# Performance work log

Measured on AMD Instinct MI355X. Metric: run time of the kernel, lower is better.

Reference implementation:

```python
import jax, jax.numpy as jnp
import numpy as np

H, O, E, V = 128, 128, 512, 34
B, T, L = 64, 2048, 256


def _lstm(x, wih, whh, bih, bhh):
    # x: [T, B, Din] -> outputs [T, B, H]; PyTorch gate order i, f, g, o
    n = whh.shape[1]
    h0 = jnp.zeros((x.shape[1], n), x.dtype)
    b = bih + bhh
    def step(carry, xt):
        h, c = carry
        g = xt @ wih.T + h @ whh.T + b
        i, f, gg, o = jnp.split(g, 4, axis=-1)
        c = jax.nn.sigmoid(f) * c + jax.nn.sigmoid(i) * jnp.tanh(gg)
        h = jax.nn.sigmoid(o) * jnp.tanh(c)
        return (h, c), h
    _, ys = jax.lax.scan(step, (h0, h0), x)
    return ys


def _conv1d_s2(x, w, b):
    # x: [B, Cin, T], w: [Cout, Cin, 2], kernel=2 stride=2 valid
    y = jax.lax.conv_general_dilated(x, w, (2,), 'VALID', dimension_numbers=('NCH', 'OIH', 'NCH'))
    return y + b[None, :, None]


def setup_inputs():
    key = jax.random.key(0)
    ctr = [0]
    def mk(shape, s=0.05):
        ctr[0] += 1
        return jax.random.normal(jax.random.fold_in(key, ctr[0]), shape, dtype=jnp.float32) * s
    inp = {}
    inp['utter'] = mk((B, T, 40), 1.0)
    inp['targets'] = jax.random.randint(jax.random.fold_in(key, 999), (B, L), 0, V)
    inp['wih_f'] = mk((4 * H, 40)); inp['whh_f'] = mk((4 * H, H)); inp['bih_f'] = mk((4 * H,)); inp['bhh_f'] = mk((4 * H,))
    inp['wih_r'] = mk((4 * H, 40)); inp['whh_r'] = mk((4 * H, H)); inp['bih_r'] = mk((4 * H,)); inp['bhh_r'] = mk((4 * H,))
    inp['c1w'] = mk((H, 2 * H, 2)); inp['c1b'] = mk((H,))
    inp['wih1'] = mk((4 * H, H)); inp['whh1'] = mk((4 * H, H)); inp['bih1'] = mk((4 * H,)); inp['bhh1'] = mk((4 * H,))
    inp['c2w'] = mk((H, H, 2)); inp['c2b'] = mk((H,))
    inp['wih2'] = mk((4 * H, H)); inp['whh2'] = mk((4 * H, H)); inp['bih2'] = mk((4 * H,)); inp['bhh2'] = mk((4 * H,))
    inp['kw'] = mk((O, H)); inp['kb'] = mk((O,)); inp['vw'] = mk((O, H)); inp['vb'] = mk((O,))
    inp['wihd'] = mk((4 * O, O + E)); inp['whhd'] = mk((4 * O, O)); inp['bihd'] = mk((4 * O,)); inp['bhhd'] = mk((4 * O,))
    inp['w1'] = mk((V, O)); inp['b1'] = mk((V,)); inp['w2'] = mk((V, O)); inp['b2'] = mk((V,))
    inp['w3'] = mk((V, V)); inp['b3'] = mk((V,))
    inp['emb'] = mk((V, E), 1.0)
    inp['sh0'] = mk((B, O)); inp['sc0'] = mk((B, O))
    return inp


def _forward(utter, targets, wih_f, whh_f, bih_f, bhh_f, wih_r, whh_r, bih_r, bhh_r,
             c1w, c1b, wih1, whh1, bih1, bhh1, c2w, c2b, wih2, whh2, bih2, bhh2,
             kw, kb, vw, vb, wihd, whhd, bihd, bhhd, w1, b1, w2, b2, w3, b3,
             emb, sh0, sc0):
    # ---- Listener (encoder) ----
    x = jnp.transpose(utter, (1, 0, 2))            # [T, B, 40]
    fwd = _lstm(x, wih_f, whh_f, bih_f, bhh_f)
    bwd = _lstm(x[::-1], wih_r, whh_r, bih_r, bhh_r)[::-1]
    h = jnp.concatenate([fwd, bwd], axis=-1)       # [T, B, 2H]
    h = jnp.transpose(h, (1, 2, 0))                # [B, 2H, T]
    h = _conv1d_s2(h, c1w, c1b)                    # [B, H, T/2]
    h = jnp.transpose(h, (2, 0, 1))                # [T/2, B, H]
    h = _lstm(h, wih1, whh1, bih1, bhh1)
    h = jnp.transpose(h, (1, 2, 0))
    h = _conv1d_s2(h, c2w, c2b)                    # [B, H, T/4]
    h = jnp.transpose(h, (2, 0, 1))
    h = _lstm(h, wih2, whh2, bih2, bhh2)
    h = jnp.transpose(h, (1, 0, 2))                # [B, T/4, H]
    hk = h @ kw.T + kb                              # [B, T/4, O]
    hv = h @ vw.T + vb
    # ---- Speller (decoder) ----
    ys = jnp.transpose(emb[targets], (1, 0, 2))[:-1]   # [L-1, B, E]
    mask = jnp.ones((utter.shape[0], hk.shape[1]), utter.dtype)  # all full-length
    bd = bihd + bhhd
    def step(carry, y_in):
        c, sh, sc = carry
        g = jnp.concatenate([y_in, c], axis=1) @ wihd.T + sh @ whhd.T + bd
        i, f, gg, o = jnp.split(g, 4, axis=-1)
        sc_n = jax.nn.sigmoid(f) * sc + jax.nn.sigmoid(i) * jnp.tanh(gg)
        sh_n = jax.nn.sigmoid(o) * jnp.tanh(sc_n)
        # NOTE: original attends with the cell state sc (faithful to source)
        att = jax.nn.softmax(jnp.einsum('btd,bd->bt', hk, sc_n), axis=1) * mask
        att = att / jnp.sum(att, axis=1, keepdims=True)
        c_n = jnp.einsum('bt,btd->bd', att, hv)
        out = jax.nn.relu(sh_n @ w1.T + b1 + c_n @ w2.T + b2)
        out = jax.nn.softmax(out @ w3.T + b3, axis=1)
        return (c_n, sh_n, sc_n), out
    c0 = jnp.zeros_like(sh0)
    _, preds = jax.lax.scan(step, (c0, sh0, sc0), ys)
    return jnp.transpose(preds, (1, 0, 2))         # [B, L-1, V]


def reference(utter, targets, wih_f, whh_f, bih_f, bhh_f, wih_r, whh_r, bih_r, bhh_r,
              c1w, c1b, wih1, whh1, bih1, bhh1, c2w, c2b, wih2, whh2, bih2, bhh2,
              kw, kb, vw, vb, wihd, whhd, bihd, bhhd, w1, b1, w2, b2, w3, b3,
              emb, sh0, sc0):
    return _forward(utter, targets, wih_f, whh_f, bih_f, bhh_f, wih_r, whh_r, bih_r, bhh_r,
                    c1w, c1b, wih1, whh1, bih1, bhh1, c2w, c2b, wih2, whh2, bih2, bhh2,
                    kw, kb, vw, vb, wihd, whhd, bihd, bhhd, w1, b1, w2, b2, w3, b3,
                    emb, sh0, sc0)
```

## Files before the change

### kernel.cpp

```cpp
#include <hip/hip_runtime.h>

typedef _Float16 half_t;
typedef _Float16 __attribute__((ext_vector_type(2))) half2_t;

__device__ __forceinline__ float fdot2_(half2_t a, half2_t b, float c) {
#if __has_builtin(__builtin_amdgcn_fdot2)
    return __builtin_amdgcn_fdot2(a, b, c, false);
#else
    return c + (float)a[0] * (float)b[0] + (float)a[1] * (float)b[1];
#endif
}
__device__ __forceinline__ half2_t h2(float a, float b) {
    half2_t r; r[0] = (half_t)a; r[1] = (half_t)b; return r;
}
__device__ __forceinline__ half2_t bc2(unsigned int u) {
    return __builtin_bit_cast(half2_t, u);
}
__device__ __forceinline__ unsigned int pk2(float a, float b) {
    return __builtin_bit_cast(unsigned int, h2(a, b));
}
__device__ __forceinline__ float sigm(float x) { return 1.0f / (1.0f + __expf(-x)); }
__device__ __forceinline__ float tanh_(float x) { return 1.0f - 2.0f / (1.0f + __expf(2.0f * x)); }
__device__ __forceinline__ unsigned int packbf2(float a, float b) {
    unsigned int ua = __float_as_uint(a);
    ua = (ua + 0x7fffu + ((ua >> 16) & 1u)) >> 16;
    unsigned int ub = __float_as_uint(b);
    ub = (ub + 0x7fffu + ((ub >> 16) & 1u)) >> 16;
    return ua | (ub << 16);
}
__device__ __forceinline__ float blo(unsigned int u) { return __uint_as_float(u << 16); }
__device__ __forceinline__ float bhi(unsigned int u) { return __uint_as_float(u & 0xffff0000u); }

__global__ __launch_bounds__(512, 1) void lstm1_k(
    const float* __restrict__ utter,
    const float* __restrict__ wih_f, const float* __restrict__ whh_f,
    const float* __restrict__ bih_f, const float* __restrict__ bhh_f,
    const float* __restrict__ wih_r, const float* __restrict__ whh_r,
    const float* __restrict__ bih_r, const float* __restrict__ bhh_r,
    unsigned short* __restrict__ Hf, unsigned short* __restrict__ Hr)
{
    const int tid = threadIdx.x;
    const int b   = blockIdx.x & 63;
    const int dir = blockIdx.x >> 6;
    const float* wih = dir ? wih_r : wih_f;
    const float* whh = dir ? whh_r : whh_f;
    const float* bih = dir ? bih_r : bih_f;
    const float* bhh = dir ? bhh_r : bhh_f;
    unsigned short* Hout = dir ? Hr : Hf;

    __shared__ float acts[512];
    __shared__ __align__(16) half_t h_h[128];
    __shared__ __align__(16) half_t x2[2][8][48];
    __shared__ __align__(16) float ring[8][128];

    const int j = tid;
    const int gt = tid >> 7;
    unsigned int wr2[64];
    {
        const float4* wp = reinterpret_cast<const float4*>(whh + j * 128);
#pragma unroll
        for (int m = 0; m < 32; ++m) {
            float4 v = wp[m];
            wr2[2 * m]     = pk2(v.x, v.y);
            wr2[2 * m + 1] = pk2(v.z, v.w);
        }
    }
    unsigned int wx2[20];
    {
        const float4* xp = reinterpret_cast<const float4*>(wih + j * 40);
#pragma unroll
        for (int q = 0; q < 10; ++q) {
            float4 v = xp[q];
            wx2[2 * q]     = pk2(v.x, v.y);
            wx2[2 * q + 1] = pk2(v.z, v.w);
        }
    }
    const float bias = bih[j] + bhh[j];
    float c = 0.0f;
    if (tid < 128) h_h[tid] = (half_t)0.0f;
    const int xs = tid / 40, xc = tid % 40;
    if (tid < 320) {
        int tt0 = dir ? (2047 - xs) : xs;
        x2[0][xs][xc] = (half_t)utter[((size_t)b * 2048 + tt0) * 40 + xc];
    }
    __syncthreads();

    for (int tc = 0; tc < 2048; tc += 8) {
        const int ph = (tc >> 3) & 1;
        float xreg = 0.0f;
        if (tid < 320) {
            int tn = tc + 8 + xs; if (tn > 2047) tn = 2047;
            int ttn = dir ? (2047 - tn) : tn;
            xreg = utter[((size_t)b * 2048 + ttn) * 40 + xc];
        }
#pragma unroll
        for (int s = 0; s < 8; ++s) {
            float g0 = bias, g1 = 0.f, g2 = 0.f, g3 = 0.f;
            {
                const uint4* x4p = reinterpret_cast<const uint4*>(&x2[ph][s][0]);
#pragma unroll
                for (int q = 0; q < 5; ++q) {
                    uint4 u = x4p[q];
                    g0 = fdot2_(bc2(wx2[4 * q]),     bc2(u.x), g0);
                    g1 = fdot2_(bc2(wx2[4 * q + 1]), bc2(u.y), g1);
                    g2 = fdot2_(bc2(wx2[4 * q + 2]), bc2(u.z), g2);
                    g3 = fdot2_(bc2(wx2[4 * q + 3]), bc2(u.w), g3);
                }
                const uint4* h4p = reinterpret_cast<const uint4*>(h_h);
#pragma unroll
                for (int q = 0; q < 16; ++q) {
                    uint4 u = h4p[q];
                    g0 = fdot2_(bc2(wr2[4 * q]),     bc2(u.x), g0);
                    g1 = fdot2_(bc2(wr2[4 * q + 1]), bc2(u.y), g1);
                    g2 = fdot2_(bc2(wr2[4 * q + 2]), bc2(u.z), g2);
                    g3 = fdot2_(bc2(wr2[4 * q + 3]), bc2(u.w), g3);
                }
            }
            float g = (g0 + g1) + (g2 + g3);
            acts[j] = (gt == 2) ? tanh_(g) : sigm(g);
            __syncthreads();
            if (s == 7 && tid < 320)
                x2[ph ^ 1][xs][xc] = (half_t)xreg;
            if (tid < 128) {
                float i_ = acts[tid];
                float f_ = acts[128 + tid];
                float g_ = acts[256 + tid];
                float o_ = acts[384 + tid];
                c = f_ * c + i_ * g_;
                float hh = o_ * tanh_(c);
                h_h[tid] = (half_t)hh;
                ring[s][tid] = hh;
            }
            __syncthreads();
        }
        {
            int s2 = tid >> 6, pr = tid & 63;
            int t = tc + s2;
            int tt = dir ? (2047 - t) : t;
            unsigned int v = pk2(ring[s2][2 * pr], ring[s2][2 * pr + 1]);
            reinterpret_cast<unsigned int*>(Hout)[((size_t)tt * 64 + b) * 64 + pr] = v;
        }
    }
}

__global__ __launch_bounds__(512, 1) void lstm_k(
    const unsigned short* __restrict__ Ph,
    const float* __restrict__ whh,
    void* __restrict__ Hout, int T, int outHalf)
{
    const int tid = threadIdx.x;
    const int b = blockIdx.x;
    const int j = tid;
    const int gt = tid >> 7;
    __shared__ float acts[512];
    __shared__ __align__(16) half_t h_h[128];
    __shared__ __align__(16) float ring[8][128];
    unsigned int wr2[64];
    {
        const float4* wp = reinterpret_cast<const float4*>(whh + j * 128);
#pragma unroll
        for (int m = 0; m < 32; ++m) {
            float4 v = wp[m];
            wr2[2 * m]     = pk2(v.x, v.y);
            wr2[2 * m + 1] = pk2(v.z, v.w);
        }
    }
    float c = 0.0f;
    if (tid < 128) h_h[tid] = (half_t)0.0f;
    const size_t pbase = (size_t)b * T;
    float pcur[8], pnext[8];
#pragma unroll
    for (int s = 0; s < 8; ++s)
        pcur[s] = (float)__builtin_bit_cast(half_t, Ph[(pbase + s) * 512 + j]);
    __syncthreads();

    for (int tc = 0; tc < T; tc += 8) {
#pragma unroll
        for (int s = 0; s < 8; ++s) {
            int tn = tc + 8 + s; if (tn > T - 1) tn = T - 1;
            pnext[s] = (float)__builtin_bit_cast(half_t, Ph[(pbase + tn) * 512 + j]);
        }
#pragma unroll
        for (int s = 0; s < 8; ++s) {
            float g0 = pcur[s], g1 = 0.f, g2 = 0.f, g3 = 0.f;
            const uint4* h4p = reinterpret_cast<const uint4*>(h_h);
#pragma unroll
            for (int q = 0; q < 16; ++q) {
                uint4 u = h4p[q];
                g0 = fdot2_(bc2(wr2[4 * q]),     bc2(u.x), g0);
                g1 = fdot2_(bc2(wr2[4 * q + 1]), bc2(u.y), g1);
                g2 = fdot2_(bc2(wr2[4 * q + 2]), bc2(u.z), g2);
                g3 = fdot2_(bc2(wr2[4 * q + 3]), bc2(u.w), g3);
            }
            float g = (g0 + g1) + (g2 + g3);
            acts[j] = (gt == 2) ? tanh_(g) : sigm(g);
            __syncthreads();
            if (tid < 128) {
                float i_ = acts[tid];
                float f_ = acts[128 + tid];
                float g_ = acts[256 + tid];
                float o_ = acts[384 + tid];
                c = f_ * c + i_ * g_;
                float hh = o_ * tanh_(c);
                h_h[tid] = (half_t)hh;
                ring[s][tid] = hh;
            }
            __syncthreads();
        }
        {
            int s2 = tid >> 6, pr = tid & 63;
            int t = tc + s2;
            if (outHalf) {
                unsigned int v = pk2(ring[s2][2 * pr], ring[s2][2 * pr + 1]);
                reinterpret_cast<unsigned int*>(Hout)[((size_t)t * 64 + b) * 64 + pr] = v;
            } else {
                float2 v = make_float2(ring[s2][2 * pr], ring[s2][2 * pr + 1]);
                *reinterpret_cast<float2*>(
                    &reinterpret_cast<float*>(Hout)[((size_t)t * 64 + b) * 128 + 2 * pr]) = v;
            }
        }
#pragma unroll
        for (int s = 0; s < 8; ++s) pcur[s] = pnext[s];
    }
}

template <int CIN>
__global__ __launch_bounds__(128) void conv_k(
    const unsigned short* __restrict__ HA, const unsigned short* __restrict__ HB,
    const float* __restrict__ W, const float* __restrict__ bias,
    float* __restrict__ out, int Tout)
{
    __shared__ __align__(16) float xin[64 * CIN];
    const int b = blockIdx.x;
    const int t0 = blockIdx.y * 32;
    const int tid = threadIdx.x;
    for (int idx = tid; idx < 64 * CIN; idx += 128) {
        int tl = idx / CIN, ci = idx % CIN;
        int tau = t0 * 2 + tl;
        unsigned short u;
        if constexpr (CIN == 256) {
            u = (ci < 128) ? HA[(size_t)tau * 8192 + b * 128 + ci]
                           : HB[(size_t)tau * 8192 + b * 128 + (ci - 128)];
        } else {
            u = HA[(size_t)tau * 8192 + b * 128 + ci];
        }
        xin[idx] = (float)__builtin_bit_cast(half_t, u);
    }
    __syncthreads();
    const int co = tid;
    float acc[32];
#pragma unroll
    for (int u = 0; u < 32; ++u) acc[u] = 0.0f;
    const float4* Wrow4 = reinterpret_cast<const float4*>(W + (size_t)co * 2 * CIN);
    const float4* xin4 = reinterpret_cast<const float4*>(xin);
    for (int c4 = 0; c4 < CIN / 4; ++c4) {
        float4 wA = Wrow4[2 * c4];
        float4 wB = Wrow4[2 * c4 + 1];
#pragma unroll
        for (int u = 0; u < 32; ++u) {
            float4 x0 = xin4[(2 * u) * (CIN / 4) + c4];
            float4 x1 = xin4[(2 * u + 1) * (CIN / 4) + c4];
            acc[u] += wA.x * x0.x + wA.y * x1.x + wA.z * x0.y + wA.w * x1.y
                    + wB.x * x0.z + wB.y * x1.z + wB.z * x0.w + wB.w * x1.w;
        }
    }
    float bs = bias[co];
#pragma unroll
    for (int u = 0; u < 32; ++u)
        out[((size_t)b * Tout + t0 + u) * 128 + co] = acc[u] + bs;
}

__global__ __launch_bounds__(256) void gemm_k(
    const float* __restrict__ A, const float* __restrict__ W, int ldw,
    const float* __restrict__ bias1, const float* __restrict__ bias2,
    void* __restrict__ C, int M, int N, int K, int mode, int Tdim)
{
    __shared__ __align__(16) float As[16][68];
    __shared__ __align__(16) float Ws[16][68];
    const int tid = threadIdx.x;
    const int m0 = blockIdx.x * 64, n0 = blockIdx.y * 64;
    const int kk = tid & 15, mm = tid >> 4;
    const int tm = tid & 15, tn = tid >> 4;
    float acc[4][4];
#pragma unroll
    for (int i = 0; i < 4; ++i)
#pragma unroll
        for (int jj = 0; jj < 4; ++jj) acc[i][jj] = 0.0f;

    for (int k0 = 0; k0 < K; k0 += 16) {
#pragma unroll
        for (int r = 0; r < 4; ++r) {
            As[kk][mm + 16 * r] = A[(size_t)(m0 + mm + 16 * r) * K + k0 + kk];
            Ws[kk][mm + 16 * r] = W[(size_t)(n0 + mm + 16 * r) * ldw + k0 + kk];
        }
        __syncthreads();
#pragma unroll
        for (int q = 0; q < 16; ++q) {
            float4 a = reinterpret_cast<const float4*>(&As[q][0])[tm];
            float4 w = reinterpret_cast<const float4*>(&Ws[q][0])[tn];
            acc[0][0] += a.x * w.x; acc[0][1] += a.x * w.y; acc[0][2] += a.x * w.z; acc[0][3] += a.x * w.w;
            acc[1][0] += a.y * w.x; acc[1][1] += a.y * w.y; acc[1][2] += a.y * w.z; acc[1][3] += a.y * w.w;
            acc[2][0] += a.z * w.x; acc[2][1] += a.z * w.y; acc[2][2] += a.z * w.z; acc[2][3] += a.z * w.w;
            acc[3][0] += a.w * w.x; acc[3][1] += a.w * w.y; acc[3][2] += a.w * w.z; acc[3][3] += a.w * w.w;
        }
        __syncthreads();
    }
    float bv[4];
#pragma unroll
    for (int jj = 0; jj < 4; ++jj) {
        int n = n0 + tn * 4 + jj;
        float v = 0.0f;
        if (bias1) v += bias1[n];
        if (bias2) v += bias2[n];
        bv[jj] = v;
    }
#pragma unroll
    for (int i = 0; i < 4; ++i) {
        int m = m0 + tm * 4 + i;
#pragma unroll
        for (int jj = 0; jj < 4; ++jj) {
            int n = n0 + tn * 4 + jj;
            float v = acc[i][jj] + bv[jj];
            if (mode == 0) {
                ((float*)C)[(size_t)m * N + n] = v;
            } else if (mode == 1) {
                int bb = m & 63, tt = m >> 6;
                ((float*)C)[((size_t)bb * N + n) * Tdim + tt] = v;
            } else {
                ((unsigned short*)C)[(size_t)m * N + n] =
                    __builtin_bit_cast(unsigned short, (half_t)v);
            }
        }
    }
}

__global__ __launch_bounds__(512) void packemb_k(
    const int* __restrict__ targets, const float* __restrict__ emb,
    float* __restrict__ Ypack)
{
    int m = blockIdx.x;
    int l = m >> 6, b = m & 63;
    int tgt = targets[b * 256 + l];
    Ypack[(size_t)m * 512 + threadIdx.x] = emb[(size_t)tgt * 512 + threadIdx.x];
}

__global__ __launch_bounds__(256) void packq_k(
    const float* __restrict__ src, unsigned int* __restrict__ dst,
    int srcCols, int colOff, int nq, int rows)
{
    int g = blockIdx.x * 256 + threadIdx.x;
    if (g >= rows * nq * 4) return;
    int k = g & 3, t = g >> 2;
    int j = t % rows, q = t / rows;
    int p = q * 4 + k;
    const float* s = src + (size_t)j * srcCols + colOff + 2 * p;
    dst[g] = pk2(s[0], s[1]);
}

__global__ __launch_bounds__(1024) void packhv2_k(
    const float* __restrict__ hvT, unsigned int* __restrict__ hvq)
{
    int b = blockIdx.x;
    for (int it = 0; it < 32; ++it) {
        int idx = it * 1024 + threadIdx.x;
        int tq = idx >> 7, d = idx & 127;
        const float* s = hvT + ((size_t)b * 128 + d) * 512 + 2 * tq;
        hvq[(size_t)b * 32768 + idx] = packbf2(s[0], s[1]);
    }
}

__global__ __launch_bounds__(512, 1) void decoder_k(
    const float* __restrict__ Yp,
    const unsigned int* __restrict__ Wd,
    const float* __restrict__ hk,
    const unsigned int* __restrict__ hvq,
    const float* __restrict__ sh0, const float* __restrict__ sc0,
    float* __restrict__ SHs, float* __restrict__ Cs)
{
    __shared__ unsigned int hk_lds[512][66];
    __shared__ float acts[512];
    __shared__ float pfl[512];
    __shared__ __align__(16) half_t sh_h[128];
    __shared__ __align__(16) float sc_f[128];
    __shared__ __align__(16) half_t c_h[128];
    __shared__ __align__(16) float att[512];
    __shared__ float red[8];

    const int tid = threadIdx.x;
    const int b = blockIdx.x;
    const int gt = tid >> 7;

    uint4 wh[16];
    {
        const uint4* W4 = reinterpret_cast<const uint4*>(Wd);
#pragma unroll
        for (int q = 0; q < 16; ++q) wh[q] = W4[q * 512 + tid];
    }
    const uint4* Wc4 = reinterpret_cast<const uint4*>(Wd) + 8192;

    {
        const float4* hp = reinterpret_cast<const float4*>(hk + ((size_t)tid * 64 + b) * 128);
#pragma unroll
        for (int q = 0; q < 32; ++q) {
            float4 v = hp[q];
            hk_lds[tid][2 * q]     = packbf2(v.x, v.y);
            hk_lds[tid][2 * q + 1] = packbf2(v.z, v.w);
        }
    }
    float sc_r = 0.0f;
    if (tid < 128) {
        sh_h[tid] = (half_t)sh0[b * 128 + tid];
        sc_r = sc0[b * 128 + tid];
        sc_f[tid] = sc_r;
        c_h[tid] = (half_t)0.0f;
    }
    __syncthreads();

    const int wid = tid >> 6, lane = tid & 63;
    const int g4 = tid >> 7, d = tid & 127;
    const unsigned int* hvp = hvq + (size_t)b * 32768 + (size_t)(g4 * 64) * 128 + d;
    const float2* att2 = reinterpret_cast<const float2*>(att);
    float yp_cur = Yp[(size_t)b * 512 + tid];

    for (int l = 0; l < 255; ++l) {
        int lnxt = (l + 1 < 255) ? (l + 1) : l;
        float yp_nxt = Yp[((size_t)lnxt * 64 + b) * 512 + tid];
        {
            float g0 = yp_cur, g1 = 0.f, g2 = 0.f, g3 = 0.f;
            const uint4* s4 = reinterpret_cast<const uint4*>(sh_h);
#pragma unroll
            for (int q = 0; q < 16; ++q) {
                uint4 u = s4[q];
                g0 = fdot2_(bc2(wh[q].x), bc2(u.x), g0);
                g1 = fdot2_(bc2(wh[q].y), bc2(u.y), g1);
                g2 = fdot2_(bc2(wh[q].z), bc2(u.z), g2);
                g3 = fdot2_(bc2(wh[q].w), bc2(u.w), g3);
            }
            const uint4* c4 = reinterpret_cast<const uint4*>(c_h);
#pragma unroll
            for (int q = 0; q < 16; ++q) {
                uint4 w = Wc4[q * 512 + tid];
                uint4 u = c4[q];
                g0 = fdot2_(bc2(w.x), bc2(u.x), g0);
                g1 = fdot2_(bc2(w.y), bc2(u.y), g1);
                g2 = fdot2_(bc2(w.z), bc2(u.z), g2);
                g3 = fdot2_(bc2(w.w), bc2(u.w), g3);
            }
            float g = (g0 + g1) + (g2 + g3);
            acts[tid] = (gt == 2) ? tanh_(g) : sigm(g);
        }
        __syncthreads();
        if (tid < 128) {
            float i_ = acts[tid];
            float f_ = acts[128 + tid];
            float g_ = acts[256 + tid];
            float o_ = acts[384 + tid];
            sc_r = f_ * sc_r + i_ * g_;
            float hh = o_ * tanh_(sc_r);
            sh_h[tid] = (half_t)hh;
            sc_f[tid] = sc_r;
            SHs[((size_t)l * 64 + b) * 128 + tid] = hh;
        }
        __syncthreads();
        {
            float e0 = 0.f, e1 = 0.f, e2 = 0.f, e3 = 0.f;
            const uint2* hkr = reinterpret_cast<const uint2*>(&hk_lds[tid][0]);
            const float4* sc4 = reinterpret_cast<const float4*>(sc_f);
#pragma unroll
            for (int q = 0; q < 32; ++q) {
                uint2 u = hkr[q];
                float4 s = sc4[q];
                e0 += blo(u.x) * s.x; e1 += bhi(u.x) * s.y;
                e2 += blo(u.y) * s.z; e3 += bhi(u.y) * s.w;
            }
            float p = __expf((e0 + e1) + (e2 + e3));
            att[tid] = p;
            float ps = p;
#pragma unroll
            for (int off = 32; off; off >>= 1) ps += __shfl_xor(ps, off);
            if (lane == 0) red[wid] = ps;
        }
        __syncthreads();
        {
            float a0 = 0.f, a1 = 0.f;
#pragma unroll 8
            for (int i = 0; i < 64; i += 2) {
                unsigned int u0 = hvp[(size_t)i * 128];
                unsigned int u1 = hvp[(size_t)(i + 1) * 128];
                float2 w0 = att2[g4 * 64 + i];
                float2 w1 = att2[g4 * 64 + i + 1];
                a0 += blo(u0) * w0.x + bhi(u0) * w0.y;
                a1 += blo(u1) * w1.x + bhi(u1) * w1.y;
            }
            pfl[tid] = a0 + a1;
        }
        __syncthreads();
        if (tid < 128) {
            float S = ((red[0] + red[1]) + (red[2] + red[3]))
                    + ((red[4] + red[5]) + (red[6] + red[7]));
            float cv = (pfl[tid] + pfl[128 + tid] + pfl[256 + tid] + pfl[384 + tid]) / S;
            c_h[tid] = (half_t)cv;
            Cs[((size_t)l * 64 + b) * 128 + tid] = cv;
        }
        yp_cur = yp_nxt;
        __syncthreads();
    }
}

__global__ __launch_bounds__(256) void mlp_k(
    const float* __restrict__ SHs, const float* __restrict__ Cs,
    const float* __restrict__ w1, const float* __restrict__ b1,
    const float* __restrict__ w2, const float* __restrict__ b2,
    const float* __restrict__ w3, const float* __restrict__ b3,
    float* __restrict__ out)
{
    __shared__ float o_l[4][34];
    const int sub = threadIdx.x >> 6, lane = threadIdx.x & 63;
    const int m = blockIdx.x * 4 + sub;
    const int l = m >> 6, b = m & 63;
    if (lane < 34) {
        float o1 = b1[lane] + b2[lane];
        const float4* w1r = reinterpret_cast<const float4*>(w1 + lane * 128);
        const float4* w2r = reinterpret_cast<const float4*>(w2 + lane * 128);
        const float4* sh4 = reinterpret_cast<const float4*>(SHs + (size_t)m * 128);
        const float4* c4  = reinterpret_cast<const float4*>(Cs + (size_t)m * 128);
#pragma unroll 8
        for (int q = 0; q < 32; ++q) {
            float4 a = w1r[q], h = sh4[q], w = w2r[q], cc = c4[q];
            o1 += a.x * h.x + a.y * h.y + a.z * h.z + a.w * h.w
                + w.x * cc.x + w.y * cc.y + w.z * cc.z + w.w * cc.w;
        }
        o_l[sub][lane] = fmaxf(o1, 0.0f);
    }
    __syncthreads();
    if (lane < 34) {
        float zz = b3[lane];
        const float* w3r = w3 + lane * 34;
        for (int v = 0; v < 34; ++v) zz += w3r[v] * o_l[sub][v];
        __syncthreads();
        o_l[sub][lane] = zz;
        __syncthreads();
        float zm = o_l[sub][0];
        for (int v = 1; v < 34; ++v) zm = fmaxf(zm, o_l[sub][v]);
        float Ssum = 0.0f;
        for (int v = 0; v < 34; ++v) Ssum += __expf(o_l[sub][v] - zm);
        out[((size_t)b * 255 + l) * 34 + lane] = __expf(zz - zm) / Ssum;
    }
}

extern "C" void kernel_launch(void* const* d_in, const int* in_sizes, int n_in,
                              void* d_out, int out_size, void* d_ws, size_t ws_size,
                              hipStream_t stream) {
    (void)in_sizes; (void)n_in; (void)out_size; (void)ws_size;
    const float* utter = (const float*)d_in[0];
    const int*   targets = (const int*)d_in[1];
    const float* wih_f = (const float*)d_in[2];
    const float* whh_f = (const float*)d_in[3];
    const float* bih_f = (const float*)d_in[4];
    const float* bhh_f = (const float*)d_in[5];
    const float* wih_r = (const float*)d_in[6];
    const float* whh_r = (const float*)d_in[7];
    const float* bih_r = (const float*)d_in[8];
    const float* bhh_r = (const float*)d_in[9];
    const float* c1w = (const float*)d_in[10];
    const float* c1b = (const float*)d_in[11];
    const float* wih1 = (const float*)d_in[12];
    const float* whh1 = (const float*)d_in[13];
    const float* bih1 = (const float*)d_in[14];
    const float* bhh1 = (const float*)d_in[15];
    const float* c2w = (const float*)d_in[16];
    const float* c2b = (const float*)d_in[17];
    const float* wih2 = (const float*)d_in[18];
    const float* whh2 = (const float*)d_in[19];
    const float* bih2 = (const float*)d_in[20];
    const float* bhh2 = (const float*)d_in[21];
    const float* kw = (const float*)d_in[22];
    const float* kb = (const float*)d_in[23];
    const float* vw = (const float*)d_in[24];
    const float* vb = (const float*)d_in[25];
    const float* wihd = (const float*)d_in[26];
    const float* whhd = (const float*)d_in[27];
    const float* bihd = (const float*)d_in[28];
    const float* bhhd = (const float*)d_in[29];
    const float* w1 = (const float*)d_in[30];
    const float* b1 = (const float*)d_in[31];
    const float* w2 = (const float*)d_in[32];
    const float* b2 = (const float*)d_in[33];
    const float* w3 = (const float*)d_in[34];
    const float* b3 = (const float*)d_in[35];
    const float* emb = (const float*)d_in[36];
    const float* sh0 = (const float*)d_in[37];
    const float* sc0 = (const float*)d_in[38];

    char* ws = (char*)d_ws;
    const size_t MB = 1ull << 20;
    unsigned int* Wd = (unsigned int*)(ws + 0);

    unsigned short* Hf_h   = (unsigned short*)(ws + 1 * MB);
    unsigned short* Hr_h   = (unsigned short*)(ws + 33 * MB);
    float*          conv1o = (float*)(ws + 65 * MB);
    unsigned short* P2_h   = (unsigned short*)(ws + 1 * MB);
    unsigned short* H2_h   = (unsigned short*)(ws + 65 * MB);
    float*          conv2o = (float*)(ws + 81 * MB);
    unsigned short* P3_h   = (unsigned short*)(ws + 97 * MB);
    float*          H3     = (float*)(ws + 1 * MB);
    float*          hkb    = (float*)(ws + 17 * MB);
    float*          hvT    = (float*)(ws + 33 * MB);
    unsigned int*   hvq    = (unsigned int*)(ws + 49 * MB);
    float*          Ypack  = (float*)(ws + 57 * MB);
    float*          Yp     = (float*)(ws + 89 * MB);
    float*          SHsave = (float*)(ws + 121 * MB);
    float*          Csave  = (float*)(ws + 130 * MB);

    packq_k<<<128, 256, 0, stream>>>(whhd, Wd + 0,     128, 0,   16, 512);
    packq_k<<<128, 256, 0, stream>>>(wihd, Wd + 32768, 640, 512, 16, 512);

    lstm1_k<<<128, 512, 0, stream>>>(utter, wih_f, whh_f, bih_f, bhh_f,
                                     wih_r, whh_r, bih_r, bhh_r, Hf_h, Hr_h);
    conv_k<256><<<dim3(64, 32), 128, 0, stream>>>(Hf_h, Hr_h, c1w, c1b, conv1o, 1024);
    gemm_k<<<dim3(1024, 8), 256, 0, stream>>>(conv1o, wih1, 128, bih1, bhh1,
                                              P2_h, 65536, 512, 128, 2, 0);
    lstm_k<<<64, 512, 0, stream>>>(P2_h, whh1, H2_h, 1024, 1);
    conv_k<128><<<dim3(64, 16), 128, 0, stream>>>(H2_h, nullptr, c2w, c2b, conv2o, 512);
    gemm_k<<<dim3(512, 8), 256, 0, stream>>>(conv2o, wih2, 128, bih2, bhh2,
                                             P3_h, 32768, 512, 128, 2, 0);
    lstm_k<<<64, 512, 0, stream>>>(P3_h, whh2, H3, 512, 0);
    gemm_k<<<dim3(512, 2), 256, 0, stream>>>(H3, kw, 128, kb, nullptr,
                                             hkb, 32768, 128, 128, 0, 0);
    gemm_k<<<dim3(512, 2), 256, 0, stream>>>(H3, vw, 128, vb, nullptr,
                                             hvT, 32768, 128, 128, 1, 512);
    packhv2_k<<<64, 1024, 0, stream>>>(hvT, hvq);
    packemb_k<<<16320, 512, 0, stream>>>(targets, emb, Ypack);
    gemm_k<<<dim3(255, 8), 256, 0, stream>>>(Ypack, wihd, 640, bihd, bhhd,
                                             Yp, 16320, 512, 512, 0, 0);
    decoder_k<<<64, 512, 0, stream>>>(Yp, Wd, hkb, hvq, sh0, sc0, SHsave, Csave);
    mlp_k<<<4080, 256, 0, stream>>>(SHsave, Csave, w1, b1, w2, b2, w3, b3, (float*)d_out);
}
```

Baseline: 5.133 ms.

## Interleave LSTM gates across lanes and combine via shuffles, dropping one barrier per step

The encoder LSTM kernels now map the four gates of each hidden unit to four adjacent lanes and exchange activations with lane shuffles, instead of writing all 512 activations to shared memory and synchronising before 128 threads do the cell update. The hidden state is double-buffered in shared memory, which removes one __syncthreads per timestep and the acts round-trip on the serial recurrence. Recurrent and input weights are pre-packed to fp16 in an interleaved layout by a new packw_k kernel, and the input-projection GEMM gets a new output mode that writes gate-interleaved order. The first bidirectional LSTM is also split into two launches, one per direction, which adds packing and launch overhead.

New measurement: 6.868 ms. 1.34x slower.

```diff
diff --git a/kernel.cpp b/kernel.cpp
--- a/kernel.cpp
+++ b/kernel.cpp
@@ -31,53 +31,49 @@
 __device__ __forceinline__ float blo(unsigned int u) { return __uint_as_float(u << 16); }
 __device__ __forceinline__ float bhi(unsigned int u) { return __uint_as_float(u & 0xffff0000u); }
 
+__global__ __launch_bounds__(256) void packw_k(
+    const float* __restrict__ src, unsigned int* __restrict__ dst, int cols, int nq)
+{
+    int g = blockIdx.x * 256 + threadIdx.x;
+    if (g >= 512 * nq * 4) return;
+    int k = g & 3, t = g >> 2;
+    int tid = t & 511, q = t >> 9;
+    int r = (tid & 3) * 128 + (tid >> 2);
+    int col = (q * 4 + k) * 2;
+    dst[g] = pk2(src[(size_t)r * cols + col], src[(size_t)r * cols + col + 1]);
+}
+
 __global__ __launch_bounds__(512, 1) void lstm1_k(
     const float* __restrict__ utter,
-    const float* __restrict__ wih_f, const float* __restrict__ whh_f,
-    const float* __restrict__ bih_f, const float* __restrict__ bhh_f,
-    const float* __restrict__ wih_r, const float* __restrict__ whh_r,
-    const float* __restrict__ bih_r, const float* __restrict__ bhh_r,
-    unsigned short* __restrict__ Hf, unsigned short* __restrict__ Hr)
+    const unsigned int* __restrict__ Wh,
+    const unsigned int* __restrict__ Wx,
+    const float* __restrict__ bih, const float* __restrict__ bhh,
+    unsigned short* __restrict__ Hout, int dir)
 {
     const int tid = threadIdx.x;
-    const int b   = blockIdx.x & 63;
-    const int dir = blockIdx.x >> 6;
-    const float* wih = dir ? wih_r : wih_f;
-    const float* whh = dir ? whh_r : whh_f;
-    const float* bih = dir ? bih_r : bih_f;
-    const float* bhh = dir ? bhh_r : bhh_f;
-    unsigned short* Hout = dir ? Hr : Hf;
-
-    __shared__ float acts[512];
-    __shared__ __align__(16) half_t h_h[128];
+    const int b = blockIdx.x;
+    const int j = tid >> 2, gate = tid & 3;
+
+    __shared__ __align__(16) half_t h_h[2][128];
     __shared__ __align__(16) half_t x2[2][8][48];
     __shared__ __align__(16) float ring[8][128];
 
-    const int j = tid;
-    const int gt = tid >> 7;
-    unsigned int wr2[64];
+    uint4 wh[16];
     {
-        const float4* wp = reinterpret_cast<const float4*>(whh + j * 128);
-#pragma unroll
-        for (int m = 0; m < 32; ++m) {
-            float4 v = wp[m];
-            wr2[2 * m]     = pk2(v.x, v.y);
-            wr2[2 * m + 1] = pk2(v.z, v.w);
-        }
-    }
-    unsigned int wx2[20];
+        const uint4* W4 = reinterpret_cast<const uint4*>(Wh);
+#pragma unroll
+        for (int q = 0; q < 16; ++q) wh[q] = W4[q * 512 + tid];
+    }
+    uint4 wx[5];
     {
-        const float4* xp = reinterpret_cast<const float4*>(wih + j * 40);
-#pragma unroll
-        for (int q = 0; q < 10; ++q) {
-            float4 v = xp[q];
-            wx2[2 * q]     = pk2(v.x, v.y);
-            wx2[2 * q + 1] = pk2(v.z, v.w);
-        }
-    }
-    const float bias = bih[j] + bhh[j];
+        const uint4* W4 = reinterpret_cast<const uint4*>(Wx);
+#pragma unroll
+        for (int q = 0; q < 5; ++q) wx[q] = W4[q * 512 + tid];
+    }
+    const int r = gate * 128 + j;
+    const float bias = bih[r] + bhh[r];
     float c = 0.0f;
-    if (tid < 128) h_h[tid] = (half_t)0.0f;
+    if (tid < 128) { h_h[0][tid] = (half_t)0.0f; }
     const int xs = tid / 40, xc = tid % 40;
     if (tid < 320) {
         int tt0 = dir ? (2047 - xs) : xs;
@@ -95,42 +91,41 @@
         }
 #pragma unroll
         for (int s = 0; s < 8; ++s) {
+            const int hb = (tc + s) & 1;
             float g0 = bias, g1 = 0.f, g2 = 0.f, g3 = 0.f;
             {
                 const uint4* x4p = reinterpret_cast<const uint4*>(&x2[ph][s][0]);
 #pragma unroll
                 for (int q = 0; q < 5; ++q) {
                     uint4 u = x4p[q];
-                    g0 = fdot2_(bc2(wx2[4 * q]),     bc2(u.x), g0);
-                    g1 = fdot2_(bc2(wx2[4 * q + 1]), bc2(u.y), g1);
-                    g2 = fdot2_(bc2(wx2[4 * q + 2]), bc2(u.z), g2);
-                    g3 = fdot2_(bc2(wx2[4 * q + 3]), bc2(u.w), g3);
+                    g0 = fdot2_(bc2(wx[q].x), bc2(u.x), g0);
+                    g1 = fdot2_(bc2(wx[q].y), bc2(u.y), g1);
+                    g2 = fdot2_(bc2(wx[q].z), bc2(u.z), g2);
+                    g3 = fdot2_(bc2(wx[q].w), bc2(u.w), g3);
                 }
-                const uint4* h4p = reinterpret_cast<const uint4*>(h_h);
+                const uint4* h4p = reinterpret_cast<const uint4*>(&h_h[hb][0]);
 #pragma unroll
                 for (int q = 0; q < 16; ++q) {
                     uint4 u = h4p[q];
-                    g0 = fdot2_(bc2(wr2[4 * q]),     bc2(u.x), g0);
-                    g1 = fdot2_(bc2(wr2[4 * q + 1]), bc2(u.y), g1);
-                    g2 = fdot2_(bc2(wr2[4 * q + 2]), bc2(u.z), g2);
-                    g3 = fdot2_(bc2(wr2[4 * q + 3]), bc2(u.w), g3);
+                    g0 = fdot2_(bc2(wh[q].x), bc2(u.x), g0);
+                    g1 = fdot2_(bc2(wh[q].y), bc2(u.y), g1);
+                    g2 = fdot2_(bc2(wh[q].z), bc2(u.z), g2);
+                    g3 = fdot2_(bc2(wh[q].w), bc2(u.w), g3);
                 }
             }
             float g = (g0 + g1) + (g2 + g3);
-            acts[j] = (gt == 2) ? tanh_(g) : sigm(g);
-            __syncthreads();
+            float act = (gate == 2) ? tanh_(g) : sigm(g);
+            float f_ = __shfl_xor(act, 1);
+            float gg = __shfl_xor(act, 2);
+            float o_ = __shfl_xor(act, 3);
+            c = f_ * c + act * gg;
+            float hh = o_ * tanh_(c);
+            if (gate == 0) {
+                h_h[hb ^ 1][j] = (half_t)hh;
+                ring[s][j] = hh;
+            }
             if (s == 7 && tid < 320)
                 x2[ph ^ 1][xs][xc] = (half_t)xreg;
-            if (tid < 128) {
-                float i_ = acts[tid];
-                float f_ = acts[128 + tid];
-                float g_ = acts[256 + tid];
-                float o_ = acts[384 + tid];
-                c = f_ * c + i_ * g_;
-                float hh = o_ * tanh_(c);
-                h_h[tid] = (half_t)hh;
-                ring[s][tid] = hh;
-            }
             __syncthreads();
         }
         {
@@ -145,65 +140,58 @@
 
 __global__ __launch_bounds__(512, 1) void lstm_k(
     const unsigned short* __restrict__ Ph,
-    const float* __restrict__ whh,
+    const unsigned int* __restrict__ Wh,
     void* __restrict__ Hout, int T, int outHalf)
 {
     const int tid = threadIdx.x;
     const int b = blockIdx.x;
-    const int j = tid;
-    const int gt = tid >> 7;
-    __shared__ float acts[512];
-    __shared__ __align__(16) half_t h_h[128];
+    const int j = tid >> 2, gate = tid & 3;
+    __shared__ __align__(16) half_t h_h[2][128];
     __shared__ __align__(16) float ring[8][128];
-    unsigned int wr2[64];
+    uint4 wh[16];
     {
-        const float4* wp = reinterpret_cast<const float4*>(whh + j * 128);
-#pragma unroll
-        for (int m = 0; m < 32; ++m) {
-            float4 v = wp[m];
-            wr2[2 * m]     = pk2(v.x, v.y);
-            wr2[2 * m + 1] = pk2(v.z, v.w);
-        }
+        const uint4* W4 = reinterpret_cast<const uint4*>(Wh);
+#pragma unroll
+        for (int q = 0; q < 16; ++q) wh[q] = W4[q * 512 + tid];
     }
     float c = 0.0f;
-    if (tid < 128) h_h[tid] = (half_t)0.0f;
+    if (tid < 128) h_h[0][tid] = (half_t)0.0f;
     const size_t pbase = (size_t)b * T;
     float pcur[8], pnext[8];
 #pragma unroll
     for (int s = 0; s < 8; ++s)
-        pcur[s] = (float)__builtin_bit_cast(half_t, Ph[(pbase + s) * 512 + j]);
+        pcur[s] = (float)__builtin_bit_cast(half_t, Ph[(pbase + s) * 512 + tid]);
     __syncthreads();
 
     for (int tc = 0; tc < T; tc += 8) {
 #pragma unroll
         for (int s = 0; s < 8; ++s) {
             int tn = tc + 8 + s; if (tn > T - 1) tn = T - 1;
-            pnext[s] = (float)__builtin_bit_cast(half_t, Ph[(pbase + tn) * 512 + j]);
+            pnext[s] = (float)__builtin_bit_cast(half_t, Ph[(pbase + tn) * 512 + tid]);
         }
 #pragma unroll
         for (int s = 0; s < 8; ++s) {
+            const int hb = (tc + s) & 1;
             float g0 = pcur[s], g1 = 0.f, g2 = 0.f, g3 = 0.f;
-            const uint4* h4p = reinterpret_cast<const uint4*>(h_h);
+            const uint4* h4p = reinterpret_cast<const uint4*>(&h_h[hb][0]);
 #pragma unroll
             for (int q = 0; q < 16; ++q) {
                 uint4 u = h4p[q];
-                g0 = fdot2_(bc2(wr2[4 * q]),     bc2(u.x), g0);
-                g1 = fdot2_(bc2(wr2[4 * q + 1]), bc2(u.y), g1);
-                g2 = fdot2_(bc2(wr2[4 * q + 2]), bc2(u.z), g2);
-                g3 = fdot2_(bc2(wr2[4 * q + 3]), bc2(u.w), g3);
+                g0 = fdot2_(bc2(wh[q].x), bc2(u.x), g0);
+                g1 = fdot2_(bc2(wh[q].y), bc2(u.y), g1);
+                g2 = fdot2_(bc2(wh[q].z), bc2(u.z), g2);
+                g3 = fdot2_(bc2(wh[q].w), bc2(u.w), g3);
             }
             float g = (g0 + g1) + (g2 + g3);
-            acts[j] = (gt == 2) ? tanh_(g) : sigm(g);
-            __syncthreads();
-            if (tid < 128) {
-                float i_ = acts[tid];
-                float f_ = acts[128 + tid];
-                float g_ = acts[256 + tid];
-                float o_ = acts[384 + tid];
-                c = f_ * c + i_ * g_;
-                float hh = o_ * tanh_(c);
-                h_h[tid] = (half_t)hh;
-                ring[s][tid] = hh;
+            float act = (gate == 2) ? tanh_(g) : sigm(g);
+            float f_ = __shfl_xor(act, 1);
+            float gg = __shfl_xor(act, 2);
+            float o_ = __shfl_xor(act, 3);
+            c = f_ * c + act * gg;
+            float hh = o_ * tanh_(c);
+            if (gate == 0) {
+                h_h[hb ^ 1][j] = (half_t)hh;
+                ring[s][j] = hh;
             }
             __syncthreads();
         }
@@ -326,8 +314,11 @@
             } else if (mode == 1) {
                 int bb = m & 63, tt = m >> 6;
                 ((float*)C)[((size_t)bb * N + n) * Tdim + tt] = v;
+            } else if (mode == 2) {
+                ((unsigned short*)C)[(size_t)m * N + n] =
+                    __builtin_bit_cast(unsigned short, (half_t)v);
             } else {
-                ((unsigned short*)C)[(size_t)m * N + n] =
+                ((unsigned short*)C)[(size_t)m * 512 + (n & 127) * 4 + (n >> 7)] =
                     __builtin_bit_cast(unsigned short, (half_t)v);
             }
         }
@@ -594,7 +585,14 @@
 
     char* ws = (char*)d_ws;
     const size_t MB = 1ull << 20;
-    unsigned int* Wd = (unsigned int*)(ws + 0);
+    unsigned int* W = (unsigned int*)(ws + 0);
+    unsigned int* Wd   = W + 0;
+    unsigned int* Wl1f = W + 65536;
+    unsigned int* Wl1r = W + 98304;
+    unsigned int* Wl2  = W + 131072;
+    unsigned int* Wl3  = W + 163840;
+    unsigned int* Wxf  = W + 196608;
+    unsigned int* Wxr  = W + 206848;
 
     unsigned short* Hf_h   = (unsigned short*)(ws + 1 * MB);
     unsigned short* Hr_h   = (unsigned short*)(ws + 33 * MB);
@@ -614,17 +612,23 @@
 
     packq_k<<<128, 256, 0, stream>>>(whhd, Wd + 0,     128, 0,   16, 512);
     packq_k<<<128, 256, 0, stream>>>(wihd, Wd + 32768, 640, 512, 16, 512);
-
-    lstm1_k<<<128, 512, 0, stream>>>(utter, wih_f, whh_f, bih_f, bhh_f,
-                                     wih_r, whh_r, bih_r, bhh_r, Hf_h, Hr_h);
+    packw_k<<<128, 256, 0, stream>>>(whh_f, Wl1f, 128, 16);
+    packw_k<<<128, 256, 0, stream>>>(whh_r, Wl1r, 128, 16);
+    packw_k<<<128, 256, 0, stream>>>(whh1, Wl2, 128, 16);
+    packw_k<<<128, 256, 0, stream>>>(whh2, Wl3, 128, 16);
+    packw_k<<<40, 256, 0, stream>>>(wih_f, Wxf, 40, 5);
+    packw_k<<<40, 256, 0, stream>>>(wih_r, Wxr, 40, 5);
+
+    lstm1_k<<<64, 512, 0, stream>>>(utter, Wl1f, Wxf, bih_f, bhh_f, Hf_h, 0);
+    lstm1_k<<<64, 512, 0, stream>>>(utter, Wl1r, Wxr, bih_r, bhh_r, Hr_h, 1);
     conv_k<256><<<dim3(64, 32), 128, 0, stream>>>(Hf_h, Hr_h, c1w, c1b, conv1o, 1024);
     gemm_k<<<dim3(1024, 8), 256, 0, stream>>>(conv1o, wih1, 128, bih1, bhh1,
-                                              P2_h, 65536, 512, 128, 2, 0);
-    lstm_k<<<64, 512, 0, stream>>>(P2_h, whh1, H2_h, 1024, 1);
+                                              P2_h, 65536, 512, 128, 3, 0);
+    lstm_k<<<64, 512, 0, stream>>>(P2_h, Wl2, H2_h, 1024, 1);
     conv_k<128><<<dim3(64, 16), 128, 0, stream>>>(H2_h, nullptr, c2w, c2b, conv2o, 512);
     gemm_k<<<dim3(512, 8), 256, 0, stream>>>(conv2o, wih2, 128, bih2, bhh2,
-                                             P3_h, 32768, 512, 128, 2, 0);
-    lstm_k<<<64, 512, 0, stream>>>(P3_h, whh2, H3, 512, 0);
+                                             P3_h, 32768, 512, 128, 3, 0);
+    lstm_k<<<64, 512, 0, stream>>>(P3_h, Wl3, H3, 512, 0);
     gemm_k<<<dim3(512, 2), 256, 0, stream>>>(H3, kw, 128, kb, nullptr,
                                              hkb, 32768, 128, 128, 0, 0);
     gemm_k<<<dim3(512, 2), 256, 0, stream>>>(H3, vw, 128, vb, nullptr,
```
